# Kernel tuning notes

Hardware: AMD Instinct MI355X
Metric: run time of the kernel (lower is better)

The kernel has to match this reference:

```python
import jax, jax.numpy as jnp
import numpy as np

N = 40000   # nodes
E = 500000  # edges
H = 2       # attention heads
C = 128     # d_graph_layer (in==out per layer)
L = 3       # n_graph_layer
G = 800     # graphs in batch
FIN = 56    # 2 * N_atom_features
NEG = 0.2   # leaky relu slope (PyG GATConv default)


def setup_inputs() -> dict:
    key = jax.random.key(0)
    ks = jax.random.split(key, 20)
    f32 = jnp.float32
    x = jax.random.normal(ks[0], (N, FIN), f32)
    edge_index = jax.random.randint(ks[1], (2, E), 0, N, jnp.int32)
    edge_attr = jax.random.uniform(ks[2], (E, 2), f32)
    valid = (jax.random.uniform(ks[3], (N, 2)) > 0.5).astype(f32)
    batch_idx = jnp.sort(jax.random.randint(ks[4], (N,), 0, G, jnp.int32))
    s = lambda k, shp, fan: jax.random.normal(k, shp, f32) / np.sqrt(fan).astype(np.float32)
    W_emb = s(ks[5], (FIN, C), FIN)
    Wg = s(ks[6], (L, C, H * C), C)           # per-layer GAT linear
    att_src = s(ks[7], (L, H, C), C)
    att_dst = s(ks[8], (L, H, C), C)
    We = s(ks[9], (L, 1, H * C), 1)           # edge_dim=1 projection
    att_e = s(ks[10], (L, H, C), C)
    bg = jnp.zeros((L, C), f32)
    gw = s(ks[11], (L, 2 * C, 1), 2 * C)      # gate linear
    gb = jnp.zeros((L, 1), f32)
    fc_w0 = s(ks[12], (2 * C, 128), 2 * C); fc_b0 = jnp.zeros((128,), f32)
    fc_w1 = s(ks[13], (128, 128), 128); fc_b1 = jnp.zeros((128,), f32)
    fc_w2 = s(ks[14], (128, 128), 128); fc_b2 = jnp.zeros((128,), f32)
    fc_w3 = s(ks[15], (128, 2), 128); fc_b3 = jnp.zeros((2,), f32)
    mu = jnp.array(0.5, f32)
    dev = jnp.array(1.0, f32)
    return dict(x=x, edge_index=edge_index, edge_attr=edge_attr, valid=valid,
                batch_idx=batch_idx, mu=mu, dev=dev, W_emb=W_emb, Wg=Wg,
                att_src=att_src, att_dst=att_dst, We=We, att_e=att_e, bg=bg,
                gw=gw, gb=gb, fc_w0=fc_w0, fc_b0=fc_b0, fc_w1=fc_w1, fc_b1=fc_b1,
                fc_w2=fc_w2, fc_b2=fc_b2, fc_w3=fc_w3, fc_b3=fc_b3)


def _seg_softmax(logits, seg, n):
    # softmax over incoming edges grouped by destination node
    m = jax.ops.segment_max(logits, seg, num_segments=n)
    e = jnp.exp(logits - m[seg])
    s = jax.ops.segment_sum(e, seg, num_segments=n)
    return e / (s[seg] + 1e-16)


def _gat_gate(h, src, dst, ea, Wk, a_s, a_d, Wek, a_e, bk, gwk, gbk):
    # edge-conditioned multi-head GAT with gated residual (concat=False -> head mean)
    n = h.shape[0]
    hh = (h @ Wk).reshape(n, H, C)                      # [N,H,C]
    ls = (hh * a_s[None]).sum(-1)                        # [N,H]
    ld = (hh * a_d[None]).sum(-1)
    eh = (ea @ Wek).reshape(-1, H, C)                    # [E,H,C]
    le = (eh * a_e[None]).sum(-1)                        # [E,H]
    logit = jax.nn.leaky_relu(ls[src] + ld[dst] + le, NEG)
    alpha = _seg_softmax(logit, dst, n)                  # [E,H]
    out = jax.ops.segment_sum(alpha[:, :, None] * hh[src], dst, num_segments=n)
    out = out.mean(1) + bk                               # head-average, [N,C]
    z = jax.nn.sigmoid(jnp.concatenate([h, out], -1) @ gwk + gbk)
    return z * h + (1.0 - z) * jax.nn.relu(out)


def reference(x, edge_index, edge_attr, valid, batch_idx, mu, dev, W_emb, Wg,
              att_src, att_dst, We, att_e, bg, gw, gb, fc_w0, fc_b0, fc_w1,
              fc_b1, fc_w2, fc_b2, fc_w3, fc_b3):
    src, dst = edge_index[0], edge_index[1]
    h = x @ W_emb
    a1 = edge_attr[:, 0:1]
    a2 = jnp.exp(-(edge_attr[:, 1:2] - mu) ** 2 / dev) + a1  # RBF + covalent
    for k in range(L):  # small fixed layer count
        h1 = _gat_gate(h, src, dst, a1, Wg[k], att_src[k], att_dst[k], We[k], att_e[k], bg[k], gw[k], gb[k])
        h2 = _gat_gate(h, src, dst, a2, Wg[k], att_src[k], att_dst[k], We[k], att_e[k], bg[k], gw[k], gb[k])
        h = h2 - h1
    gl = jax.ops.segment_sum(h * valid[:, 0:1], batch_idx, num_segments=G)
    gp = jax.ops.segment_sum(h * valid[:, 1:2], batch_idx, num_segments=G)
    o = jnp.concatenate([gl, gp], -1)                    # [G, 2C]
    o = jax.nn.relu(o @ fc_w0 + fc_b0)
    o = jax.nn.relu(o @ fc_w1 + fc_b1)
    o = jax.nn.relu(o @ fc_w2 + fc_b2)
    o = o @ fc_w3 + fc_b3
    return jnp.stack([o[:, 0], jnp.exp(o[:, 1])], axis=1)
```

## Files before the change

### kernel.cpp

```cpp
#include <hip/hip_runtime.h>
#include <hip/hip_fp16.h>
#include <math.h>

#define NN 40000
#define EE 500000
#define CC 128
#define GG 800
#define FINN 56
#define NEGS 0.2f
#define CAP 48

typedef _Float16 f16x8 __attribute__((ext_vector_type(8)));
typedef float f32x4 __attribute__((ext_vector_type(4)));

__device__ __forceinline__ float lrelu(float x) { return x > 0.f ? x : NEGS * x; }

#define WGSZ (3 * 256 * 128)
#define WESZ (128 * 64)
#define PREPN ((WGSZ + WESZ) / 256)

__global__ void k_prep(const float* __restrict__ Wg, const float* __restrict__ W_emb,
                       const float* __restrict__ We, const float* __restrict__ ate,
                       __half* __restrict__ Wt, __half* __restrict__ Wet,
                       float* __restrict__ wd, int* __restrict__ deg) {
    int gi = blockIdx.x * 256 + threadIdx.x;
    if (gi < NN) deg[gi] = 0;
    if (blockIdx.x == PREPN) {
        if (threadIdx.x < 64) {
            int lane = threadIdx.x;
            for (int idx = 0; idx < 6; ++idx) {
                const float* w = We + idx * 128;
                const float* a = ate + idx * 128;
                float p = w[lane] * a[lane] + w[lane + 64] * a[lane + 64];
                #pragma unroll
                for (int m = 32; m; m >>= 1) p += __shfl_xor(p, m);
                if (lane == 0) wd[idx] = p;
            }
        }
        return;
    }
    if (gi < WGSZ) {
        int l = gi >> 15, rem = gi & 32767;
        int c = rem >> 7, kk = rem & 127;
        Wt[gi] = __float2half_rn(Wg[l * 32768 + kk * 256 + c]);
    } else {
        int j = gi - WGSZ;
        int c = j >> 6, kk = j & 63;
        Wet[j] = (kk < FINN) ? __float2half_rn(W_emb[kk * CC + c]) : __half(0.f);
    }
}

__global__ void k_scatter(const int* __restrict__ ei, const float* __restrict__ ea,
                          const float* __restrict__ mu, const float* __restrict__ dev,
                          int* __restrict__ deg, int4* __restrict__ slab) {
    int e = blockIdx.x * 256 + threadIdx.x;
    if (e >= EE) return;
    int s = ei[e], d = ei[EE + e];
    float a1 = ea[2 * e];
    float xx = ea[2 * e + 1] - mu[0];
    float a2 = __expf(-xx * xx / dev[0]) + a1;
    int p = atomicAdd(&deg[d], 1);
    if (p < CAP) slab[d * CAP + p] = make_int4(s, __float_as_int(a1), __float_as_int(a2), 0);
}

__global__ __launch_bounds__(128) void k_embed16(
    const float* __restrict__ x, const __half* __restrict__ Wet,
    float* __restrict__ h, __half* __restrict__ h16) {
    int tid = threadIdx.x;
    int wave = tid >> 6, lane = tid & 63;
    int row0 = blockIdx.x * 16;
    int rlo = lane & 15, kgrp = lane >> 4;
    const float* xrow = x + (row0 + rlo) * FINN;
    f16x8 a0, a1;
    #pragma unroll
    for (int j = 0; j < 8; ++j) a0[j] = (_Float16)xrow[kgrp * 8 + j];
    #pragma unroll
    for (int j = 0; j < 8; ++j) {
        int k = 32 + kgrp * 8 + j;
        a1[j] = (k < FINN) ? (_Float16)xrow[k] : (_Float16)0.f;
    }
    #pragma unroll
    for (int nt = 0; nt < 4; ++nt) {
        int col = wave * 64 + nt * 16 + rlo;
        f32x4 acc = {0.f, 0.f, 0.f, 0.f};
        const __half* bbase = Wet + col * 64 + kgrp * 8;
        acc = __builtin_amdgcn_mfma_f32_16x16x32_f16(a0, *(const f16x8*)(bbase), acc, 0, 0, 0);
        acc = __builtin_amdgcn_mfma_f32_16x16x32_f16(a1, *(const f16x8*)(bbase + 32), acc, 0, 0, 0);
        #pragma unroll
        for (int r = 0; r < 4; ++r) {
            int row = row0 + kgrp * 4 + r;
            h[row * CC + col] = acc[r];
            h16[row * CC + col] = __float2half_rn(acc[r]);
        }
    }
}

__global__ __launch_bounds__(256) void k_gemm16(
    const __half* __restrict__ h16, const __half* __restrict__ Wt,
    const float* __restrict__ as_, const float* __restrict__ ad_,
    __half* __restrict__ hh16, float* __restrict__ lsld) {
    __shared__ float2 red[16][4];
    int tid = threadIdx.x;
    int wave = tid >> 6, lane = tid & 63;
    int row0 = blockIdx.x * 16;
    int rlo = lane & 15, kgrp = lane >> 4;
    f16x8 afrag[4];
    const __half* abase = h16 + (row0 + rlo) * CC + kgrp * 8;
    #pragma unroll
    for (int ks = 0; ks < 4; ++ks) afrag[ks] = *(const f16x8*)(abase + ks * 32);
    int head = wave >> 1;
    const float* as_h = as_ + head * CC;
    const float* ad_h = ad_ + head * CC;
    float psum[4] = {0.f, 0.f, 0.f, 0.f}, pdsum[4] = {0.f, 0.f, 0.f, 0.f};
    #pragma unroll
    for (int nt = 0; nt < 4; ++nt) {
        int col = wave * 64 + nt * 16 + rlo;
        f32x4 acc = {0.f, 0.f, 0.f, 0.f};
        const __half* bbase = Wt + col * CC + kgrp * 8;
        #pragma unroll
        for (int ks = 0; ks < 4; ++ks) {
            f16x8 bfrag = *(const f16x8*)(bbase + ks * 32);
            acc = __builtin_amdgcn_mfma_f32_16x16x32_f16(afrag[ks], bfrag, acc, 0, 0, 0);
        }
        float av = as_h[col & 127], dv = ad_h[col & 127];
        #pragma unroll
        for (int r = 0; r < 4; ++r) {
            float v = acc[r];
            hh16[(row0 + kgrp * 4 + r) * 256 + col] = __float2half_rn(v);
            psum[r] += v * av;
            pdsum[r] += v * dv;
        }
    }
    #pragma unroll
    for (int r = 0; r < 4; ++r) {
        #pragma unroll
        for (int m = 1; m < 16; m <<= 1) {
            psum[r] += __shfl_xor(psum[r], m);
            pdsum[r] += __shfl_xor(pdsum[r], m);
        }
    }
    if (rlo == 0) {
        #pragma unroll
        for (int r = 0; r < 4; ++r) red[kgrp * 4 + r][wave] = make_float2(psum[r], pdsum[r]);
    }
    __syncthreads();
    if (tid < 64) {
        int row = tid >> 2, which = tid & 3;
        float v;
        if (which == 0)      v = red[row][0].x + red[row][1].x;
        else if (which == 1) v = red[row][2].x + red[row][3].x;
        else if (which == 2) v = red[row][0].y + red[row][1].y;
        else                 v = red[row][2].y + red[row][3].y;
        lsld[(row0 + row) * 4 + which] = v;
    }
}

__global__ __launch_bounds__(256) void k_attn(
    const __half* __restrict__ hh16, const float* __restrict__ hcur,
    const float* __restrict__ lsld,
    const int* __restrict__ deg, const int4* __restrict__ slab,
    const float* __restrict__ wd, const float* __restrict__ bg,
    const float* __restrict__ gw, const float* __restrict__ gb,
    float* __restrict__ hout, __half* __restrict__ h16out) {
    __shared__ float4 evM[8][32];
    __shared__ int    evS[8][32];
    int tid = threadIdx.x;
    int sub = tid & 31;
    int hw = tid >> 5;
    int n = blockIdx.x * 8 + hw;
    float wd0 = wd[0], wd1 = wd[1];
    float4 nld = *(const float4*)&lsld[n * 4];
    float ld0 = nld.z, ld1 = nld.w;
    int count = min(deg[n], CAP);
    const int4* srow = slab + n * CAP;
    int hd01 = sub >> 4;
    float s0 = 0, s1 = 0, s2 = 0, s3 = 0;
    float acc1[8] = {0,0,0,0,0,0,0,0}, acc2[8] = {0,0,0,0,0,0,0,0};
    const char* hbase = (const char*)hh16 + sub * 16;

    for (int j0 = 0; j0 < count; j0 += 32) {
        int nact = min(32, count - j0);
        float4 e4 = make_float4(0.f, 0.f, 0.f, 0.f);
        int smine = 0;
        if (j0 + sub < count) {
            int4 c = srow[j0 + sub];
            smine = c.x;
            float a1 = __int_as_float(c.y), a2 = __int_as_float(c.z);
            float2 lsv = *(const float2*)&lsld[smine * 4];
            float b0 = lsv.x + ld0, b1 = lsv.y + ld1;
            e4.x = __expf(fminf(lrelu(b0 + a1 * wd0), 80.f));
            e4.y = __expf(fminf(lrelu(b0 + a2 * wd0), 80.f));
            e4.z = __expf(fminf(lrelu(b1 + a1 * wd1), 80.f));
            e4.w = __expf(fminf(lrelu(b1 + a2 * wd1), 80.f));
            s0 += e4.x; s1 += e4.y; s2 += e4.z; s3 += e4.w;
        }
        evM[hw][sub] = e4;
        evS[hw][sub] = smine * 512;
        int npv = (nact + 3) & ~3;
        for (int jj = 0; jj < npv; jj += 4) {
            float4 emA = evM[hw][jj],     emB = evM[hw][jj + 1];
            float4 emC = evM[hw][jj + 2], emD = evM[hw][jj + 3];
            int oA = evS[hw][jj],     oB = evS[hw][jj + 1];
            int oC = evS[hw][jj + 2], oD = evS[hw][jj + 3];
            union { uint4 u; _Float16 hx[8]; } rA, rB, rC, rD;
            rA.u = *(const uint4*)(hbase + oA);
            rB.u = *(const uint4*)(hbase + oB);
            rC.u = *(const uint4*)(hbase + oC);
            rD.u = *(const uint4*)(hbase + oD);
            float eA1 = hd01 ? emA.z : emA.x, eA2 = hd01 ? emA.w : emA.y;
            float eB1 = hd01 ? emB.z : emB.x, eB2 = hd01 ? emB.w : emB.y;
            float eC1 = hd01 ? emC.z : emC.x, eC2 = hd01 ? emC.w : emC.y;
            float eD1 = hd01 ? emD.z : emD.x, eD2 = hd01 ? emD.w : emD.y;
            #pragma unroll
            for (int i = 0; i < 8; ++i) {
                float vA = (float)rA.hx[i], vB = (float)rB.hx[i];
                float vC = (float)rC.hx[i], vD = (float)rD.hx[i];
                acc1[i] += eA1 * vA; acc2[i] += eA2 * vA;
                acc1[i] += eB1 * vB; acc2[i] += eB2 * vB;
                acc1[i] += eC1 * vC; acc2[i] += eC2 * vC;
                acc1[i] += eD1 * vD; acc2[i] += eD2 * vD;
            }
        }
    }
    #pragma unroll
    for (int m = 16; m; m >>= 1) {
        s0 += __shfl_xor(s0, m); s1 += __shfl_xor(s1, m);
        s2 += __shfl_xor(s2, m); s3 += __shfl_xor(s3, m);
    }
    float d1 = (hd01 ? s2 : s0) + 1e-16f;
    float d2 = (hd01 ? s3 : s1) + 1e-16f;
    float id1 = 1.f / d1, id2 = 1.f / d2;
    int c0 = (sub & 15) * 8;
    float o1[8], o2[8];
    #pragma unroll
    for (int i = 0; i < 8; ++i) { o1[i] = acc1[i] * id1; o2[i] = acc2[i] * id2; }
    #pragma unroll
    for (int i = 0; i < 8; ++i) {
        o1[i] = 0.5f * (o1[i] + __shfl_xor(o1[i], 16)) + bg[c0 + i];
        o2[i] = 0.5f * (o2[i] + __shfl_xor(o2[i], 16)) + bg[c0 + i];
    }
    float hv[8];
    *(float4*)&hv[0] = ((const float4*)hcur)[n * 32 + (sub & 15) * 2];
    *(float4*)&hv[4] = ((const float4*)hcur)[n * 32 + (sub & 15) * 2 + 1];
    float pp1 = 0.f, pp2 = 0.f;
    if (sub < 16) {
        #pragma unroll
        for (int i = 0; i < 8; ++i) {
            pp1 += o1[i] * gw[128 + c0 + i];
            pp2 += o2[i] * gw[128 + c0 + i];
        }
    } else {
        float hp = 0.f;
        #pragma unroll
        for (int i = 0; i < 8; ++i) hp += hv[i] * gw[c0 + i];
        pp1 = hp; pp2 = hp;
    }
    #pragma unroll
    for (int m = 16; m; m >>= 1) { pp1 += __shfl_xor(pp1, m); pp2 += __shfl_xor(pp2, m); }
    float z1 = 1.f / (1.f + __expf(-(pp1 + gb[0])));
    float z2 = 1.f / (1.f + __expf(-(pp2 + gb[0])));
    if (sub < 16) {
        float r[8];
        #pragma unroll
        for (int i = 0; i < 8; ++i) {
            float g1 = z1 * hv[i] + (1.f - z1) * fmaxf(o1[i], 0.f);
            float g2 = z2 * hv[i] + (1.f - z2) * fmaxf(o2[i], 0.f);
            r[i] = g2 - g1;
        }
        ((float4*)hout)[n * 32 + (sub & 15) * 2]     = make_float4(r[0], r[1], r[2], r[3]);
        ((float4*)hout)[n * 32 + (sub & 15) * 2 + 1] = make_float4(r[4], r[5], r[6], r[7]);
        union { __half h[8]; uint4 u; } pk;
        #pragma unroll
        for (int i = 0; i < 8; ++i) pk.h[i] = __float2half_rn(r[i]);
        *(uint4*)&h16out[n * CC + c0] = pk.u;
    }
}

__global__ __launch_bounds__(128) void k_readmlp(
    const float* __restrict__ h, const float* __restrict__ valid, const int* __restrict__ batch,
    const float* __restrict__ w0, const float* __restrict__ b0,
    const float* __restrict__ w1, const float* __restrict__ b1,
    const float* __restrict__ w2, const float* __restrict__ b2,
    const float* __restrict__ w3, const float* __restrict__ b3,
    float* __restrict__ out) {
    __shared__ float cur[256];
    __shared__ float nxt[128];
    int g = blockIdx.x, t = threadIdx.x;
    int lo = 0, hi = NN;
    while (lo < hi) { int mid = (lo + hi) >> 1; if (batch[mid] < g) lo = mid + 1; else hi = mid; }
    int s = lo;
    lo = s; hi = NN;
    while (lo < hi) { int mid = (lo + hi) >> 1; if (batch[mid] < g + 1) lo = mid + 1; else hi = mid; }
    int e = lo;
    float gl = 0, gp = 0;
    for (int n = s; n < e; ++n) {
        float hv = h[n * CC + t];
        gl += hv * valid[2 * n];
        gp += hv * valid[2 * n + 1];
    }
    cur[t] = gl; cur[t + 128] = gp;
    __syncthreads();
    float ss = b0[t];
    for (int i = 0; i < 256; ++i) ss += cur[i] * w0[i * 128 + t];
    nxt[t] = fmaxf(ss, 0.f);
    __syncthreads();
    ss = b1[t];
    for (int i = 0; i < 128; ++i) ss += nxt[i] * w1[i * 128 + t];
    cur[t] = fmaxf(ss, 0.f);
    __syncthreads();
    ss = b2[t];
    for (int i = 0; i < 128; ++i) ss += cur[i] * w2[i * 128 + t];
    nxt[t] = fmaxf(ss, 0.f);
    __syncthreads();
    if (t < 2) {
        float o = b3[t];
        for (int i = 0; i < 128; ++i) o += nxt[i] * w3[i * 2 + t];
        out[g * 2 + t] = (t == 1) ? expf(o) : o;
    }
}

extern "C" void kernel_launch(void* const* d_in, const int* in_sizes, int n_in,
                              void* d_out, int out_size, void* d_ws, size_t ws_size,
                              hipStream_t stream) {
    const float* x      = (const float*)d_in[0];
    const int*   ei     = (const int*)d_in[1];
    const float* ea     = (const float*)d_in[2];
    const float* valid  = (const float*)d_in[3];
    const int*   batch  = (const int*)d_in[4];
    const float* mu     = (const float*)d_in[5];
    const float* devp   = (const float*)d_in[6];
    const float* W_emb  = (const float*)d_in[7];
    const float* Wg     = (const float*)d_in[8];
    const float* att_s  = (const float*)d_in[9];
    const float* att_d  = (const float*)d_in[10];
    const float* We     = (const float*)d_in[11];
    const float* att_e  = (const float*)d_in[12];
    const float* bg     = (const float*)d_in[13];
    const float* gw     = (const float*)d_in[14];
    const float* gb     = (const float*)d_in[15];
    const float* fw0    = (const float*)d_in[16];
    const float* fb0    = (const float*)d_in[17];
    const float* fw1    = (const float*)d_in[18];
    const float* fb1    = (const float*)d_in[19];
    const float* fw2    = (const float*)d_in[20];
    const float* fb2    = (const float*)d_in[21];
    const float* fw3    = (const float*)d_in[22];
    const float* fb3    = (const float*)d_in[23];
    float* out = (float*)d_out;

    char* p = (char*)d_ws;
    auto alloc = [&](size_t bytes) -> char* {
        char* r = p;
        p += (bytes + 255) & ~(size_t)255;
        return r;
    };
    float*  h0      = (float*)alloc((size_t)NN * CC * 4);
    float*  h1      = (float*)alloc((size_t)NN * CC * 4);
    __half* h16a    = (__half*)alloc((size_t)NN * CC * 2);
    __half* h16b    = (__half*)alloc((size_t)NN * CC * 2);
    __half* hh16    = (__half*)alloc((size_t)NN * 256 * 2);
    __half* Wt      = (__half*)alloc((size_t)3 * 256 * 128 * 2);
    __half* Wet     = (__half*)alloc((size_t)128 * 64 * 2);
    float*  lsld    = (float*)alloc((size_t)NN * 4 * 4);
    int*    deg     = (int*)alloc((size_t)NN * 4);
    int4*   slab    = (int4*)alloc((size_t)NN * CAP * 16);
    float*  wd      = (float*)alloc(256);

    k_prep<<<PREPN + 1, 256, 0, stream>>>(Wg, W_emb, We, att_e, Wt, Wet, wd, deg);
    k_scatter<<<(EE + 255) / 256, 256, 0, stream>>>(ei, ea, mu, devp, deg, slab);
    k_embed16<<<NN / 16, 128, 0, stream>>>(x, Wet, h0, h16a);

    float*  hc = h0;     float*  hn = h1;
    __half* hc16 = h16a; __half* hn16 = h16b;
    for (int k = 0; k < 3; ++k) {
        k_gemm16<<<NN / 16, 256, 0, stream>>>(hc16, Wt + (size_t)k * 32768,
                                              att_s + k * 256, att_d + k * 256, hh16, lsld);
        k_attn<<<NN / 8, 256, 0, stream>>>(hh16, hc, lsld, deg, slab,
                                           wd + k * 2, bg + k * 128, gw + k * 256, gb + k,
                                           hn, hn16);
        float* t1 = hc; hc = hn; hn = t1;
        __half* t2 = hc16; hc16 = hn16; hn16 = t2;
    }

    k_readmlp<<<GG, 128, 0, stream>>>(hc, valid, batch,
                                      fw0, fb0, fw1, fb1, fw2, fb2, fw3, fb3, out);
}
```

Before: 405.1 us.

## Stage fp16 GEMM outputs through shared memory and shrink attention gather unroll

The embed and GAT-linear kernels now write their fp16 outputs into a padded shared-memory tile and then store them to global memory as coalesced 16-byte vectors, replacing scattered 2-byte stores. The attention aggregation loop drops from four gathered neighbor rows per iteration to two, which pads fewer edges per chunk and may lower register pressure, at the cost of fewer loads in flight. The staging adds a shared-memory round trip and a barrier in the embed kernel.

After: 416.2 us. 2.7% more time.

```diff
diff --git a/kernel.cpp b/kernel.cpp
--- a/kernel.cpp
+++ b/kernel.cpp
@@ -66,6 +66,7 @@
 __global__ __launch_bounds__(128) void k_embed16(
     const float* __restrict__ x, const __half* __restrict__ Wet,
     float* __restrict__ h, __half* __restrict__ h16) {
+    __shared__ __half tile[16][136];
     int tid = threadIdx.x;
     int wave = tid >> 6, lane = tid & 63;
     int row0 = blockIdx.x * 16;
@@ -90,15 +91,23 @@
         for (int r = 0; r < 4; ++r) {
             int row = row0 + kgrp * 4 + r;
             h[row * CC + col] = acc[r];
-            h16[row * CC + col] = __float2half_rn(acc[r]);
-        }
-    }
+            tile[kgrp * 4 + r][col] = __float2half_rn(acc[r]);
+        }
+    }
+    __syncthreads();
+    int row = tid >> 3, chunk = tid & 7;
+    uint4 a = *(uint4*)&tile[row][chunk * 16];
+    uint4 b = *(uint4*)&tile[row][chunk * 16 + 8];
+    __half* dst = &h16[(row0 + row) * CC + chunk * 16];
+    *(uint4*)dst = a;
+    *(uint4*)(dst + 8) = b;
 }
 
 __global__ __launch_bounds__(256) void k_gemm16(
     const __half* __restrict__ h16, const __half* __restrict__ Wt,
     const float* __restrict__ as_, const float* __restrict__ ad_,
     __half* __restrict__ hh16, float* __restrict__ lsld) {
+    __shared__ __half tile[16][264];
     __shared__ float2 red[16][4];
     int tid = threadIdx.x;
     int wave = tid >> 6, lane = tid & 63;
@@ -126,7 +135,7 @@
         #pragma unroll
         for (int r = 0; r < 4; ++r) {
             float v = acc[r];
-            hh16[(row0 + kgrp * 4 + r) * 256 + col] = __float2half_rn(v);
+            tile[kgrp * 4 + r][col] = __float2half_rn(v);
             psum[r] += v * av;
             pdsum[r] += v * dv;
         }
@@ -144,6 +153,14 @@
         for (int r = 0; r < 4; ++r) red[kgrp * 4 + r][wave] = make_float2(psum[r], pdsum[r]);
     }
     __syncthreads();
+    {
+        int row = tid >> 4, chunk = tid & 15;
+        uint4 a = *(uint4*)&tile[row][chunk * 16];
+        uint4 b = *(uint4*)&tile[row][chunk * 16 + 8];
+        __half* dst = &hh16[(row0 + row) * 256 + chunk * 16];
+        *(uint4*)dst = a;
+        *(uint4*)(dst + 8) = b;
+    }
     if (tid < 64) {
         int row = tid >> 2, which = tid & 3;
         float v;
@@ -196,29 +213,20 @@
         }
         evM[hw][sub] = e4;
         evS[hw][sub] = smine * 512;
-        int npv = (nact + 3) & ~3;
-        for (int jj = 0; jj < npv; jj += 4) {
-            float4 emA = evM[hw][jj],     emB = evM[hw][jj + 1];
-            float4 emC = evM[hw][jj + 2], emD = evM[hw][jj + 3];
-            int oA = evS[hw][jj],     oB = evS[hw][jj + 1];
-            int oC = evS[hw][jj + 2], oD = evS[hw][jj + 3];
-            union { uint4 u; _Float16 hx[8]; } rA, rB, rC, rD;
+        int npv = (nact + 1) & ~1;
+        for (int jj = 0; jj < npv; jj += 2) {
+            float4 emA = evM[hw][jj], emB = evM[hw][jj + 1];
+            int oA = evS[hw][jj], oB = evS[hw][jj + 1];
+            union { uint4 u; _Float16 hx[8]; } rA, rB;
             rA.u = *(const uint4*)(hbase + oA);
             rB.u = *(const uint4*)(hbase + oB);
-            rC.u = *(const uint4*)(hbase + oC);
-            rD.u = *(const uint4*)(hbase + oD);
             float eA1 = hd01 ? emA.z : emA.x, eA2 = hd01 ? emA.w : emA.y;
             float eB1 = hd01 ? emB.z : emB.x, eB2 = hd01 ? emB.w : emB.y;
-            float eC1 = hd01 ? emC.z : emC.x, eC2 = hd01 ? emC.w : emC.y;
-            float eD1 = hd01 ? emD.z : emD.x, eD2 = hd01 ? emD.w : emD.y;
             #pragma unroll
             for (int i = 0; i < 8; ++i) {
                 float vA = (float)rA.hx[i], vB = (float)rB.hx[i];
-                float vC = (float)rC.hx[i], vD = (float)rD.hx[i];
                 acc1[i] += eA1 * vA; acc2[i] += eA2 * vA;
                 acc1[i] += eB1 * vB; acc2[i] += eB2 * vB;
-                acc1[i] += eC1 * vC; acc2[i] += eC2 * vC;
-                acc1[i] += eD1 * vD; acc2[i] += eD2 * vD;
             }
         }
     }
```
